# Kernel tuning notes

Hardware: AMD Instinct MI355X
Metric: run time of the kernel (lower is better)

## Reference

```python
import jax, jax.numpy as jnp
import numpy as np

N = 32768      # total points (multiple of patch_size -> no padding needed)
C = 768        # channels
H = 8          # num heads
K = 256        # patch_size (window length)
HD = C // H    # head dim = 96, divisible by 6 (3 axes * rotary pairs)
FREQ = 100.0   # rope_freq


def rope3d(x, pos):
    """Point-position RoPE: head dim split into 3 axis chunks, each rotated
    by angles pos_axis * freq**(-i/half).  x: [N,H,HD], pos: [N,3] float."""
    d_axis = HD // 3            # 32
    half = d_axis // 2          # 16
    inv_freq = FREQ ** (-jnp.arange(half, dtype=x.dtype) / half)   # [half]
    ang = pos[:, :, None] * inv_freq[None, None, :]                # [N,3,half]
    cos = jnp.cos(ang)[:, None, :, :]                              # [N,1,3,half]
    sin = jnp.sin(ang)[:, None, :, :]
    xr = x.reshape(x.shape[0], x.shape[1], 3, d_axis)              # [N,H,3,d_axis]
    x1, x2 = xr[..., :half], xr[..., half:]
    out = jnp.concatenate([x1 * cos - x2 * sin, x1 * sin + x2 * cos], axis=-1)
    return out.reshape(x.shape)


def setup_inputs() -> dict:
    key = jax.random.key(0)
    ks = jax.random.split(key, 6)
    feat = jax.random.normal(ks[0], (N, C), dtype=jnp.float32)
    grid_coord = jax.random.randint(ks[1], (N, 3), 0, 1024, dtype=jnp.int32)
    order = jax.random.permutation(ks[2], N).astype(jnp.int32)     # serialized order
    inverse = jnp.argsort(order).astype(jnp.int32)                 # its inverse
    w_qkv = jax.random.normal(ks[3], (C, 3 * C), dtype=jnp.float32) * 0.02
    b_qkv = jnp.zeros((3 * C,), dtype=jnp.float32)
    w_proj = jax.random.normal(ks[4], (C, C), dtype=jnp.float32) * 0.02
    b_proj = jnp.zeros((C,), dtype=jnp.float32)
    return {"feat": feat, "grid_coord": grid_coord, "order": order,
            "inverse": inverse, "w_qkv": w_qkv, "b_qkv": b_qkv,
            "w_proj": w_proj, "b_proj": b_proj}


def reference(feat, grid_coord, order, inverse, w_qkv, b_qkv, w_proj, b_proj):
    scale = HD ** -0.5
    P = N // K  # number of windows
    qkv = (feat @ w_qkv + b_qkv)[order]                   # gather by serialized order
    pos = grid_coord[order].astype(feat.dtype)            # [N,3]
    q, k, v = jnp.split(qkv, 3, axis=-1)
    q = rope3d(q.reshape(N, H, HD), pos)
    k = rope3d(k.reshape(N, H, HD), pos)
    v = v.reshape(N, H, HD)
    # windowed (varlen with equal patch lengths) attention
    qw = q.reshape(P, K, H, HD)
    kw = k.reshape(P, K, H, HD)
    vw = v.reshape(P, K, H, HD)
    logits = jnp.einsum('pqhd,pkhd->phqk', qw, kw) * scale
    attn = jax.nn.softmax(logits, axis=-1)
    out = jnp.einsum('phqk,pkhd->pqhd', attn, vw).reshape(N, C)
    out = out[inverse]                                    # scatter back to input order
    return out @ w_proj + b_proj
```

## Files before the change

### kernel.cpp

```cpp
#include <hip/hip_runtime.h>
#include <hip/hip_bf16.h>
#include <stdint.h>

typedef __bf16 bf16_t;
typedef __bf16 bf16x8 __attribute__((ext_vector_type(8)));
typedef __bf16 bf16x4 __attribute__((ext_vector_type(4)));
typedef float f32x4 __attribute__((ext_vector_type(4)));

template <int V> struct ic { static constexpr int value = V; };

__device__ __forceinline__ void gload_lds16(const bf16_t* g, bf16_t* l) {
  __builtin_amdgcn_global_load_lds((const __attribute__((address_space(1))) void*)g,
                                   (__attribute__((address_space(3))) void*)l, 16, 0, 0);
}

__global__ __launch_bounds__(256) void transpose_cast_k(const float* __restrict__ W,
                                                        bf16_t* __restrict__ Bt,
                                                        int KDin, int MDin) {
  __shared__ float tile[64][65];
  const int bm = blockIdx.x, bk = blockIdx.y;
  const int c = threadIdx.x & 63, r0 = threadIdx.x >> 6;
#pragma unroll
  for (int rr = 0; rr < 16; ++rr) {
    int row = rr * 4 + r0;
    tile[row][c] = W[(size_t)(bk * 64 + row) * MDin + bm * 64 + c];
  }
  __syncthreads();
#pragma unroll
  for (int rr = 0; rr < 16; ++rr) {
    int mo = rr * 4 + r0;
    Bt[(size_t)(bm * 64 + mo) * KDin + bk * 64 + c] = (bf16_t)tile[c][mo];
  }
}

__global__ __launch_bounds__(256) void gather_cast_k(const float* __restrict__ feat,
                                                     const int* __restrict__ order,
                                                     const int* __restrict__ grid_coord,
                                                     bf16_t* __restrict__ featp,
                                                     float* __restrict__ posf) {
  const int id = blockIdx.x * 256 + threadIdx.x;
  const int j = id / 192;
  const int c = (id % 192) * 4;
  const int g = order[j];
  const float4 v = *(const float4*)(feat + (size_t)g * 768 + c);
  bf16x4 o;
  o[0] = (bf16_t)v.x; o[1] = (bf16_t)v.y; o[2] = (bf16_t)v.z; o[3] = (bf16_t)v.w;
  *(bf16x4*)(featp + (size_t)j * 768 + c) = o;
  if (c == 0) {
    posf[j * 3 + 0] = (float)grid_coord[g * 3 + 0];
    posf[j * 3 + 1] = (float)grid_coord[g * 3 + 1];
    posf[j * 3 + 2] = (float)grid_coord[g * 3 + 2];
  }
}

template <int MODE, int NBX>
__global__ __launch_bounds__(512, 2) void gemm256_k(const bf16_t* __restrict__ A,
                                                    const bf16_t* __restrict__ Bt,
                                                    const float* __restrict__ bias,
                                                    bf16_t* __restrict__ Cq,
                                                    bf16_t* __restrict__ Ck,
                                                    bf16_t* __restrict__ Cv,
                                                    float* __restrict__ Cf,
                                                    const int* __restrict__ order,
                                                    const float* __restrict__ posf) {
  extern __shared__ bf16_t sm[];
  bf16_t* ldsA = sm;
  bf16_t* ldsB = sm + 4 * 8192;

  const int tid = threadIdx.x;
  const int lane = tid & 63, wave = tid >> 6;
  const int wr = wave >> 2, wc = wave & 3;
  const int lq = lane & 15, lk = lane >> 4;

  const int bid = blockIdx.x;
  const int cpx = gridDim.x >> 3;
  const int rm = (bid & 7) * cpx + (bid >> 3);
  const int by = rm / NBX, bx = rm % NBX;

  const int o0 = tid, o1 = tid + 512;
  const int r0s = o0 >> 2, ls0 = (o0 & 3) ^ ((r0s >> 1) & 3);
  const int r1s = o1 >> 2, ls1 = (o1 & 3) ^ ((r1s >> 1) & 3);
  const bf16_t* pA0 = A + (size_t)(by * 256 + r0s) * 768 + ls0 * 8;
  const bf16_t* pA1 = A + (size_t)(by * 256 + r1s) * 768 + ls1 * 8;
  const bf16_t* pB0 = Bt + (size_t)(bx * 256 + r0s) * 768 + ls0 * 8;
  const bf16_t* pB1 = Bt + (size_t)(bx * 256 + r1s) * 768 + ls1 * 8;

  auto stageA = [&](int kt) {
    bf16_t* d = ldsA + ((kt & 3) << 13);
    gload_lds16(pA0 + kt * 32, d + o0 * 8);
    gload_lds16(pA1 + kt * 32, d + o1 * 8);
  };
  auto stageB = [&](int kt) {
    bf16_t* d = ldsB + ((kt & 3) << 13);
    gload_lds16(pB0 + kt * 32, d + o0 * 8);
    gload_lds16(pB1 + kt * 32, d + o1 * 8);
  };

  const int pslot = lk ^ ((lq >> 1) & 3);

  f32x4 acc[8][4] = {};

  stageA(0); stageB(0); stageA(1); stageB(1); stageA(2); stageB(2);
  asm volatile("s_waitcnt vmcnt(8)" ::: "memory");
  __builtin_amdgcn_s_barrier();
  __builtin_amdgcn_sched_barrier(0);

  auto group = [&](int t, auto VMC, auto STGC) {
    constexpr int VM = decltype(VMC)::value;
    constexpr bool STG = decltype(STGC)::value;
    const bf16_t* Ab = ldsA + ((t & 3) << 13);
    const bf16_t* Bb = ldsB + ((t & 3) << 13);
    bf16x8 af[4], bfr[4];
#pragma unroll
    for (int m = 0; m < 4; ++m)
      af[m] = *(const bf16x8*)(Ab + (wr * 128 + m * 16 + lq) * 32 + pslot * 8);
#pragma unroll
    for (int n = 0; n < 4; ++n)
      bfr[n] = *(const bf16x8*)(Bb + (wc * 64 + n * 16 + lq) * 32 + pslot * 8);
    if constexpr (STG) stageA(t + 3);
    __builtin_amdgcn_s_barrier();
    asm volatile("s_waitcnt lgkmcnt(0)" ::: "memory");
    __builtin_amdgcn_s_setprio(1);
#pragma unroll
    for (int n = 0; n < 4; ++n)
#pragma unroll
      for (int m = 0; m < 4; ++m)
        acc[m][n] = __builtin_amdgcn_mfma_f32_16x16x32_bf16(af[m], bfr[n], acc[m][n], 0, 0, 0);
    __builtin_amdgcn_s_setprio(0);
    __builtin_amdgcn_s_barrier();
#pragma unroll
    for (int m = 0; m < 4; ++m)
      af[m] = *(const bf16x8*)(Ab + (wr * 128 + 64 + m * 16 + lq) * 32 + pslot * 8);
    if constexpr (STG) stageB(t + 3);
    if constexpr (VM == 8) asm volatile("s_waitcnt vmcnt(8)" ::: "memory");
    else if constexpr (VM == 4) asm volatile("s_waitcnt vmcnt(4)" ::: "memory");
    else if constexpr (VM == 0) asm volatile("s_waitcnt vmcnt(0)" ::: "memory");
    __builtin_amdgcn_s_barrier();
    asm volatile("s_waitcnt lgkmcnt(0)" ::: "memory");
    __builtin_amdgcn_s_setprio(1);
#pragma unroll
    for (int n = 0; n < 4; ++n)
#pragma unroll
      for (int m = 0; m < 4; ++m)
        acc[4 + m][n] = __builtin_amdgcn_mfma_f32_16x16x32_bf16(af[m], bfr[n], acc[4 + m][n], 0, 0, 0);
    __builtin_amdgcn_s_setprio(0);
    __builtin_amdgcn_s_barrier();
    __builtin_amdgcn_sched_barrier(0);
  };

  for (int t = 0; t < 21; ++t) group(t, ic<8>{}, ic<1>{});
  group(21, ic<4>{}, ic<0>{});
  group(22, ic<0>{}, ic<0>{});
  group(23, ic<-1>{}, ic<0>{});

  const int colb = bx * 256 + wc * 64;
  float bcol[4];
#pragma unroll
  for (int n = 0; n < 4; ++n) bcol[n] = bias[colb + n * 16 + lq];

  if (MODE == 0) {
    const int sec = bx / 3;
    const int coll = colb - sec * 768;
    if (sec < 2) {
      bf16_t* base = sec == 0 ? Cq : Ck;
      const int a0 = (colb % 96) >> 5;
      const int a1 = ((colb + 32) % 96) >> 5;
      const float fr = exp2f(-0.41524101186f * (float)lq);
#pragma unroll
      for (int m = 0; m < 8; ++m) {
        const int rowb = by * 256 + wr * 128 + m * 16 + lk * 4;
#pragma unroll
        for (int r = 0; r < 4; ++r) {
          const int row = rowb + r;
          float s0, c0, s1, c1;
          __sincosf(posf[row * 3 + a0] * fr, &s0, &c0);
          __sincosf(posf[row * 3 + a1] * fr, &s1, &c1);
          const float x1 = acc[m][0][r] + bcol[0], x2 = acc[m][1][r] + bcol[1];
          const float y1 = acc[m][2][r] + bcol[2], y2 = acc[m][3][r] + bcol[3];
          acc[m][0][r] = x1 * c0 - x2 * s0;
          acc[m][1][r] = x1 * s0 + x2 * c0;
          acc[m][2][r] = y1 * c1 - y2 * s1;
          acc[m][3][r] = y1 * s1 + y2 * c1;
        }
#pragma unroll
        for (int n = 0; n < 4; ++n) {
          const int col = coll + n * 16 + lq;
#pragma unroll
          for (int r = 0; r < 4; ++r)
            base[(size_t)(rowb + r) * 768 + col] = (bf16_t)acc[m][n][r];
        }
      }
    } else {
#pragma unroll
      for (int m = 0; m < 8; ++m) {
        const int rowb = by * 256 + wr * 128 + m * 16 + lk * 4;
#pragma unroll
        for (int n = 0; n < 4; ++n) {
          const int col = coll + n * 16 + lq;
          bf16x4 o;
#pragma unroll
          for (int r = 0; r < 4; ++r) o[r] = (bf16_t)(acc[m][n][r] + bcol[n]);
          *(bf16x4*)(Cv + (size_t)col * 32768 + rowb) = o;
        }
      }
    }
  } else {
#pragma unroll
    for (int m = 0; m < 8; ++m) {
      const int rowb = by * 256 + wr * 128 + m * 16 + lk * 4;
      int ro[4];
#pragma unroll
      for (int r = 0; r < 4; ++r) ro[r] = order[rowb + r];
#pragma unroll
      for (int n = 0; n < 4; ++n) {
        const int col = colb + n * 16 + lq;
#pragma unroll
        for (int r = 0; r < 4; ++r)
          Cf[(size_t)ro[r] * 768 + col] = acc[m][n][r] + bcol[n];
      }
    }
  }
}

__global__ __launch_bounds__(512, 2) void gemm_proj_k(const bf16_t* __restrict__ A,
                                                      const bf16_t* __restrict__ Bt,
                                                      const float* __restrict__ bias,
                                                      float* __restrict__ Cf,
                                                      const int* __restrict__ inverse) {
  extern __shared__ bf16_t sm[];
  bf16_t* ldsA = sm;
  bf16_t* ldsB = sm + 16384;

  const int tid = threadIdx.x;
  const int lane = tid & 63, wave = tid >> 6;
  const int wr = wave >> 2, wc = wave & 3;
  const int lq = lane & 15, lk = lane >> 4;

  const int bid = blockIdx.x;
  const int cpx = gridDim.x >> 3;
  const int rm = (bid & 7) * cpx + (bid >> 3);
  const int by = rm / 3, bx = rm % 3;

  const int rA = tid >> 2, lsA = (tid & 3) ^ ((rA >> 1) & 3);
  const int gA = inverse[by * 128 + rA];
  const bf16_t* pA = A + (size_t)gA * 768 + lsA * 8;
  const int o0 = tid, o1 = tid + 512;
  const int rB0 = o0 >> 2, lsB0 = (o0 & 3) ^ ((rB0 >> 1) & 3);
  const int rB1 = o1 >> 2, lsB1 = (o1 & 3) ^ ((rB1 >> 1) & 3);
  const bf16_t* pB0 = Bt + (size_t)(bx * 256 + rB0) * 768 + lsB0 * 8;
  const bf16_t* pB1 = Bt + (size_t)(bx * 256 + rB1) * 768 + lsB1 * 8;

  auto stage = [&](int kt) {
    const int slot = kt & 3;
    gload_lds16(pA + kt * 32, ldsA + (slot << 12) + tid * 8);
    gload_lds16(pB0 + kt * 32, ldsB + (slot << 13) + o0 * 8);
    gload_lds16(pB1 + kt * 32, ldsB + (slot << 13) + o1 * 8);
  };

  const int pslot = lk ^ ((lq >> 1) & 3);

  f32x4 acc[4][4] = {};

  stage(0); stage(1); stage(2);
  asm volatile("s_waitcnt vmcnt(6)" ::: "memory");
  __builtin_amdgcn_s_barrier();
  __builtin_amdgcn_sched_barrier(0);

  auto group = [&](int t, auto VMC, auto STGC) {
    constexpr int VM = decltype(VMC)::value;
    constexpr bool STG = decltype(STGC)::value;
    const bf16_t* Ab = ldsA + ((t & 3) << 12);
    const bf16_t* Bb = ldsB + ((t & 3) << 13);
    bf16x8 af[4], bfr[4];
#pragma unroll
    for (int m = 0; m < 4; ++m)
      af[m] = *(const bf16x8*)(Ab + (wr * 64 + m * 16 + lq) * 32 + pslot * 8);
#pragma unroll
    for (int n = 0; n < 4; ++n)
      bfr[n] = *(const bf16x8*)(Bb + (wc * 64 + n * 16 + lq) * 32 + pslot * 8);
    if constexpr (STG) stage(t + 3);
    if constexpr (VM == 6) asm volatile("s_waitcnt vmcnt(6)" ::: "memory");
    else if constexpr (VM == 3) asm volatile("s_waitcnt vmcnt(3)" ::: "memory");
    else if constexpr (VM == 0) asm volatile("s_waitcnt vmcnt(0)" ::: "memory");
    __builtin_amdgcn_s_barrier();
    asm volatile("s_waitcnt lgkmcnt(0)" ::: "memory");
    __builtin_amdgcn_sched_barrier(0);
    __builtin_amdgcn_s_setprio(1);
#pragma unroll
    for (int n = 0; n < 4; ++n)
#pragma unroll
      for (int m = 0; m < 4; ++m)
        acc[m][n] = __builtin_amdgcn_mfma_f32_16x16x32_bf16(af[m], bfr[n], acc[m][n], 0, 0, 0);
    __builtin_amdgcn_s_setprio(0);
    __builtin_amdgcn_s_barrier();
    __builtin_amdgcn_sched_barrier(0);
  };

  for (int t = 0; t < 21; ++t) group(t, ic<6>{}, ic<1>{});
  group(21, ic<3>{}, ic<0>{});
  group(22, ic<0>{}, ic<0>{});
  group(23, ic<-1>{}, ic<0>{});

  const int colb = bx * 256 + wc * 64;
  float bcol[4];
#pragma unroll
  for (int n = 0; n < 4; ++n) bcol[n] = bias[colb + n * 16 + lq];
#pragma unroll
  for (int m = 0; m < 4; ++m) {
    const int rowb = by * 128 + wr * 64 + m * 16 + lk * 4;
#pragma unroll
    for (int n = 0; n < 4; ++n) {
      const int col = colb + n * 16 + lq;
#pragma unroll
      for (int r = 0; r < 4; ++r)
        Cf[(size_t)(rowb + r) * 768 + col] = acc[m][n][r] + bcol[n];
    }
  }
}

__global__ __launch_bounds__(512) void attn_k(bf16_t* QO,
                                              const bf16_t* __restrict__ Kb,
                                              const bf16_t* __restrict__ Vt) {
  extern __shared__ bf16_t alds[];
  bf16_t* Kreg = alds;
  bf16_t* Vreg = alds + 24576;
  const int bid = blockIdx.x;
  const int h = bid & 7, p = bid >> 3;
  const int tid = threadIdx.x, lane = tid & 63, wave = tid >> 6;
  const int lq = lane & 15, lk = lane >> 4;
  const int tok0 = p * 256;
  const float scale = 0.10206207262f;
  bf16_t* pw = alds + 49152 + wave * 2048;

  bf16x8 aq[2][3];
#pragma unroll
  for (int rb = 0; rb < 2; ++rb) {
    const bf16_t* qb = QO + (size_t)(tok0 + wave * 32 + rb * 16 + lq) * 768 + h * 96 + lk * 8;
#pragma unroll
    for (int kc = 0; kc < 3; ++kc) aq[rb][kc] = *(const bf16x8*)(qb + kc * 32);
  }
  __builtin_amdgcn_sched_barrier(0);

#pragma unroll
  for (int i = 0; i < 6; ++i) {
    const int fi = i * 8 + wave;
    const int nt = fi / 3, a = fi - nt * 3;
    const bf16_t* src = Kb + (size_t)(tok0 + nt * 16 + (lane & 15)) * 768 +
                        h * 96 + a * 32 + (lane >> 4) * 8;
    gload_lds16(src, Kreg + i * 4096 + tid * 8);
  }
#pragma unroll
  for (int i = 0; i < 6; ++i) {
    const int fi = i * 8 + wave;
    const int d = (fi >> 3) * 16 + (lane & 15);
    const int tb = (fi & 7) * 32 + (lane >> 4) * 8;
    const bf16_t* src = Vt + (size_t)(h * 96 + d) * 32768 + tok0 + tb;
    gload_lds16(src, Vreg + i * 4096 + tid * 8);
  }

  asm volatile("s_waitcnt vmcnt(6)" ::: "memory");
  __builtin_amdgcn_s_barrier();

#pragma unroll
  for (int rb = 0; rb < 2; ++rb) {
    f32x4 sacc[16];
#pragma unroll
    for (int nt = 0; nt < 16; ++nt) {
      f32x4 acc = {0.f, 0.f, 0.f, 0.f};
#pragma unroll
      for (int kc = 0; kc < 3; ++kc) {
        bf16x8 bk = *(const bf16x8*)(Kreg + (size_t)((nt * 3 + kc) * 64 + lane) * 8);
        acc = __builtin_amdgcn_mfma_f32_16x16x32_bf16(aq[rb][kc], bk, acc, 0, 0, 0);
      }
      sacc[nt] = acc;
    }

    float linv[4];
#pragma unroll
    for (int r = 0; r < 4; ++r) {
      float mx = -1e30f;
#pragma unroll
      for (int nt = 0; nt < 16; ++nt) mx = fmaxf(mx, sacc[nt][r]);
      mx = fmaxf(mx, __shfl_xor(mx, 1));
      mx = fmaxf(mx, __shfl_xor(mx, 2));
      mx = fmaxf(mx, __shfl_xor(mx, 4));
      mx = fmaxf(mx, __shfl_xor(mx, 8));
      mx *= scale;
      float l = 0.f;
#pragma unroll
      for (int nt = 0; nt < 16; ++nt) {
        float e = __expf(sacc[nt][r] * scale - mx);
        sacc[nt][r] = e;
        l += e;
      }
      l += __shfl_xor(l, 1);
      l += __shfl_xor(l, 2);
      l += __shfl_xor(l, 4);
      l += __shfl_xor(l, 8);
      linv[r] = 1.f / l;
    }

    if (rb == 0) {
      asm volatile("s_waitcnt vmcnt(0)" ::: "memory");
      __builtin_amdgcn_s_barrier();
    }

    f32x4 oacc[6] = {};
#pragma unroll
    for (int hf = 0; hf < 2; ++hf) {
#pragma unroll
      for (int ntl = 0; ntl < 8; ++ntl) {
        const int nt = hf * 8 + ntl;
        const int chk = ntl * 2 + (lq >> 3);
#pragma unroll
        for (int r = 0; r < 4; ++r) {
          const int row = lk * 4 + r;
          const int phys = chk ^ (row & 7);
          pw[row * 128 + phys * 8 + (lq & 7)] = (bf16_t)sacc[nt][r];
        }
      }
#pragma unroll
      for (int kcl = 0; kcl < 4; ++kcl) {
        const int physr = (kcl * 4 + lk) ^ (lq & 7);
        bf16x8 pf = *(const bf16x8*)(pw + lq * 128 + physr * 8);
        const int kc = hf * 4 + kcl;
#pragma unroll
        for (int dt = 0; dt < 6; ++dt) {
          bf16x8 vb = *(const bf16x8*)(Vreg + (size_t)((dt * 8 + kc) * 64 + lane) * 8);
          oacc[dt] = __builtin_amdgcn_mfma_f32_16x16x32_bf16(pf, vb, oacc[dt], 0, 0, 0);
        }
      }
    }

#pragma unroll
    for (int dt = 0; dt < 6; ++dt) {
#pragma unroll
      for (int r = 0; r < 4; ++r) {
        const int row = tok0 + wave * 32 + rb * 16 + lk * 4 + r;
        QO[(size_t)row * 768 + h * 96 + dt * 16 + lq] = (bf16_t)(oacc[dt][r] * linv[r]);
      }
    }
  }
}

extern "C" void kernel_launch(void* const* d_in, const int* in_sizes, int n_in,
                              void* d_out, int out_size, void* d_ws, size_t ws_size,
                              hipStream_t stream) {
  const float* feat       = (const float*)d_in[0];
  const int*   grid_coord = (const int*)d_in[1];
  const int*   order      = (const int*)d_in[2];
  const int*   inverse    = (const int*)d_in[3];
  const float* w_qkv      = (const float*)d_in[4];
  const float* b_qkv      = (const float*)d_in[5];
  const float* w_proj     = (const float*)d_in[6];
  const float* b_proj     = (const float*)d_in[7];
  float* out = (float*)d_out;

  char* ws = (char*)d_ws;
  bf16_t* Bt1   = (bf16_t*)(ws);
  bf16_t* Bt2   = (bf16_t*)(ws + 3538944);
  bf16_t* featp = (bf16_t*)(ws + 4718592);
  bf16_t* Qb    = (bf16_t*)(ws + 55050240);
  bf16_t* Kb    = (bf16_t*)(ws + 105381888);
  bf16_t* Vt    = (bf16_t*)(ws + 155713536);
  float*  posf  = (float*)(ws + 206045184);

  static bool attr_set = false;
  if (!attr_set) {
    (void)hipFuncSetAttribute((const void*)gemm256_k<0, 9>,
                              hipFuncAttributeMaxDynamicSharedMemorySize, 131072);
    (void)hipFuncSetAttribute((const void*)gemm_proj_k,
                              hipFuncAttributeMaxDynamicSharedMemorySize, 98304);
    (void)hipFuncSetAttribute((const void*)attn_k,
                              hipFuncAttributeMaxDynamicSharedMemorySize, 131072);
    attr_set = true;
  }

  transpose_cast_k<<<dim3(36, 12), 256, 0, stream>>>(w_qkv, Bt1, 768, 2304);
  transpose_cast_k<<<dim3(12, 12), 256, 0, stream>>>(w_proj, Bt2, 768, 768);
  gather_cast_k<<<24576, 256, 0, stream>>>(feat, order, grid_coord, featp, posf);
  gemm256_k<0, 9><<<1152, 512, 131072, stream>>>(featp, Bt1, b_qkv, Qb, Kb, Vt,
                                                 nullptr, nullptr, posf);
  attn_k<<<1024, 512, 131072, stream>>>(Qb, Kb, Vt);
  gemm_proj_k<<<768, 512, 98304, stream>>>(Qb, Bt2, b_proj, out, inverse);
}
```

Before: 478.6 us.

## Restructure GEMM main loops: single-phase QKV tiles and two-k-step projection phases

The QKV GEMM loop no longer splits each k-step into two half-tile MFMA phases with separate A/B staging. It loads all eight A fragments at once and runs all 32 MFMAs between one barrier pair, which halves the barriers per k-step but needs more VGPRs for fragments. The projection GEMM now processes two k-steps per phase with a 4-slot ring, staging two tiles ahead and issuing 32 MFMAs per barrier pair. This cuts synchronisation overhead, but the prefetch depth now alternates, which can expose global-load latency.

```diff
diff --git a/kernel.cpp b/kernel.cpp
--- a/kernel.cpp
+++ b/kernel.cpp
@@ -85,73 +85,58 @@
   const bf16_t* pB0 = Bt + (size_t)(bx * 256 + r0s) * 768 + ls0 * 8;
   const bf16_t* pB1 = Bt + (size_t)(bx * 256 + r1s) * 768 + ls1 * 8;
 
-  auto stageA = [&](int kt) {
-    bf16_t* d = ldsA + ((kt & 3) << 13);
-    gload_lds16(pA0 + kt * 32, d + o0 * 8);
-    gload_lds16(pA1 + kt * 32, d + o1 * 8);
+  auto stageAB = [&](int kt) {
+    bf16_t* dA = ldsA + ((kt & 3) << 13);
+    bf16_t* dB = ldsB + ((kt & 3) << 13);
+    gload_lds16(pA0 + kt * 32, dA + o0 * 8);
+    gload_lds16(pA1 + kt * 32, dA + o1 * 8);
+    gload_lds16(pB0 + kt * 32, dB + o0 * 8);
+    gload_lds16(pB1 + kt * 32, dB + o1 * 8);
   };
-  auto stageB = [&](int kt) {
-    bf16_t* d = ldsB + ((kt & 3) << 13);
-    gload_lds16(pB0 + kt * 32, d + o0 * 8);
-    gload_lds16(pB1 + kt * 32, d + o1 * 8);
-  };
 
   const int pslot = lk ^ ((lq >> 1) & 3);
 
   f32x4 acc[8][4] = {};
 
-  stageA(0); stageB(0); stageA(1); stageB(1); stageA(2); stageB(2);
+  stageAB(0); stageAB(1); stageAB(2);
   asm volatile("s_waitcnt vmcnt(8)" ::: "memory");
   __builtin_amdgcn_s_barrier();
   __builtin_amdgcn_sched_barrier(0);
 
-  auto group = [&](int t, auto VMC, auto STGC) {
+  auto phase = [&](int t, auto VMC, auto STGC) {
     constexpr int VM = decltype(VMC)::value;
     constexpr bool STG = decltype(STGC)::value;
     const bf16_t* Ab = ldsA + ((t & 3) << 13);
     const bf16_t* Bb = ldsB + ((t & 3) << 13);
-    bf16x8 af[4], bfr[4];
-#pragma unroll
-    for (int m = 0; m < 4; ++m)
+    bf16x8 af[8], bfr[4];
+#pragma unroll
+    for (int m = 0; m < 8; ++m)
       af[m] = *(const bf16x8*)(Ab + (wr * 128 + m * 16 + lq) * 32 + pslot * 8);
 #pragma unroll
     for (int n = 0; n < 4; ++n)
       bfr[n] = *(const bf16x8*)(Bb + (wc * 64 + n * 16 + lq) * 32 + pslot * 8);
-    if constexpr (STG) stageA(t + 3);
-    __builtin_amdgcn_s_barrier();
-    asm volatile("s_waitcnt lgkmcnt(0)" ::: "memory");
-    __builtin_amdgcn_s_setprio(1);
-#pragma unroll
-    for (int n = 0; n < 4; ++n)
-#pragma unroll
-      for (int m = 0; m < 4; ++m)
-        acc[m][n] = __builtin_amdgcn_mfma_f32_16x16x32_bf16(af[m], bfr[n], acc[m][n], 0, 0, 0);
-    __builtin_amdgcn_s_setprio(0);
-    __builtin_amdgcn_s_barrier();
-#pragma unroll
-    for (int m = 0; m < 4; ++m)
-      af[m] = *(const bf16x8*)(Ab + (wr * 128 + 64 + m * 16 + lq) * 32 + pslot * 8);
-    if constexpr (STG) stageB(t + 3);
+    if constexpr (STG) stageAB(t + 3);
     if constexpr (VM == 8) asm volatile("s_waitcnt vmcnt(8)" ::: "memory");
     else if constexpr (VM == 4) asm volatile("s_waitcnt vmcnt(4)" ::: "memory");
     else if constexpr (VM == 0) asm volatile("s_waitcnt vmcnt(0)" ::: "memory");
     __builtin_amdgcn_s_barrier();
     asm volatile("s_waitcnt lgkmcnt(0)" ::: "memory");
+    __builtin_amdgcn_sched_barrier(0);
     __builtin_amdgcn_s_setprio(1);
 #pragma unroll
     for (int n = 0; n < 4; ++n)
 #pragma unroll
-      for (int m = 0; m < 4; ++m)
-        acc[4 + m][n] = __builtin_amdgcn_mfma_f32_16x16x32_bf16(af[m], bfr[n], acc[4 + m][n], 0, 0, 0);
+      for (int m = 0; m < 8; ++m)
+        acc[m][n] = __builtin_amdgcn_mfma_f32_16x16x32_bf16(af[m], bfr[n], acc[m][n], 0, 0, 0);
     __builtin_amdgcn_s_setprio(0);
     __builtin_amdgcn_s_barrier();
     __builtin_amdgcn_sched_barrier(0);
   };
 
-  for (int t = 0; t < 21; ++t) group(t, ic<8>{}, ic<1>{});
-  group(21, ic<4>{}, ic<0>{});
-  group(22, ic<0>{}, ic<0>{});
-  group(23, ic<-1>{}, ic<0>{});
+  for (int t = 0; t < 21; ++t) phase(t, ic<8>{}, ic<1>{});
+  phase(21, ic<4>{}, ic<0>{});
+  phase(22, ic<0>{}, ic<0>{});
+  phase(23, ic<-1>{}, ic<0>{});
 
   const int colb = bx * 256 + wc * 64;
   float bcol[4];
@@ -261,45 +246,45 @@
 
   f32x4 acc[4][4] = {};
 
-  stage(0); stage(1); stage(2);
-  asm volatile("s_waitcnt vmcnt(6)" ::: "memory");
-  __builtin_amdgcn_s_barrier();
-  __builtin_amdgcn_sched_barrier(0);
-
-  auto group = [&](int t, auto VMC, auto STGC) {
+  stage(0); stage(1);
+
+  auto phasep = [&](int p, auto VMC, auto STGC) {
     constexpr int VM = decltype(VMC)::value;
     constexpr bool STG = decltype(STGC)::value;
-    const bf16_t* Ab = ldsA + ((t & 3) << 12);
-    const bf16_t* Bb = ldsB + ((t & 3) << 13);
-    bf16x8 af[4], bfr[4];
-#pragma unroll
-    for (int m = 0; m < 4; ++m)
-      af[m] = *(const bf16x8*)(Ab + (wr * 64 + m * 16 + lq) * 32 + pslot * 8);
-#pragma unroll
-    for (int n = 0; n < 4; ++n)
-      bfr[n] = *(const bf16x8*)(Bb + (wc * 64 + n * 16 + lq) * 32 + pslot * 8);
-    if constexpr (STG) stage(t + 3);
+    if constexpr (STG) { stage(2 * p + 2); stage(2 * p + 3); }
     if constexpr (VM == 6) asm volatile("s_waitcnt vmcnt(6)" ::: "memory");
-    else if constexpr (VM == 3) asm volatile("s_waitcnt vmcnt(3)" ::: "memory");
     else if constexpr (VM == 0) asm volatile("s_waitcnt vmcnt(0)" ::: "memory");
     __builtin_amdgcn_s_barrier();
+    bf16x8 af[2][4], bfr[2][4];
+#pragma unroll
+    for (int hh = 0; hh < 2; ++hh) {
+      const int kt = 2 * p + hh;
+      const bf16_t* Ab = ldsA + ((kt & 3) << 12);
+      const bf16_t* Bb = ldsB + ((kt & 3) << 13);
+#pragma unroll
+      for (int m = 0; m < 4; ++m)
+        af[hh][m] = *(const bf16x8*)(Ab + (wr * 64 + m * 16 + lq) * 32 + pslot * 8);
+#pragma unroll
+      for (int n = 0; n < 4; ++n)
+        bfr[hh][n] = *(const bf16x8*)(Bb + (wc * 64 + n * 16 + lq) * 32 + pslot * 8);
+    }
     asm volatile("s_waitcnt lgkmcnt(0)" ::: "memory");
     __builtin_amdgcn_sched_barrier(0);
     __builtin_amdgcn_s_setprio(1);
 #pragma unroll
-    for (int n = 0; n < 4; ++n)
-#pragma unroll
-      for (int m = 0; m < 4; ++m)
-        acc[m][n] = __builtin_amdgcn_mfma_f32_16x16x32_bf16(af[m], bfr[n], acc[m][n], 0, 0, 0);
+    for (int hh = 0; hh < 2; ++hh)
+#pragma unroll
+      for (int n = 0; n < 4; ++n)
+#pragma unroll
+        for (int m = 0; m < 4; ++m)
+          acc[m][n] = __builtin_amdgcn_mfma_f32_16x16x32_bf16(af[hh][m], bfr[hh][n], acc[m][n], 0, 0, 0);
     __builtin_amdgcn_s_setprio(0);
     __builtin_amdgcn_s_barrier();
     __builtin_amdgcn_sched_barrier(0);
   };
 
-  for (int t = 0; t < 21; ++t) group(t, ic<6>{}, ic<1>{});
-  group(21, ic<3>{}, ic<0>{});
-  group(22, ic<0>{}, ic<0>{});
-  group(23, ic<-1>{}, ic<0>{});
+  for (int p = 0; p < 11; ++p) phasep(p, ic<6>{}, ic<1>{});
+  phasep(11, ic<0>{}, ic<0>{});
 
   const int colb = bx * 256 + wc * 64;
   float bcol[4];
```

Result: no change. 474.9 us (-0.8%).
